# Kernel tuning notes

Hardware: AMD Instinct MI355X
Metric: run time of the kernel (lower is better)

## Reference

```python
import jax, jax.numpy as jnp
import numpy as np

N_NODES = 50000
N_EDGES = 1600000


def _gcn_conv(x, src, dst, W, b, num_nodes):
    # PyG GCNConv: out = D^-1/2 (A + I) D^-1/2 (x W) + b
    h = x @ W  # transform first (in_channels >= out_channels)
    deg = jax.ops.segment_sum(jnp.ones_like(dst, dtype=h.dtype), dst,
                              num_segments=num_nodes)
    dinv = jax.lax.rsqrt(deg)  # deg >= 1 thanks to self-loops
    norm = dinv[src] * dinv[dst]  # [E+N]
    msg = h[src] * norm[:, None]  # gather + scale
    out = jax.ops.segment_sum(msg, dst, num_segments=num_nodes)
    return out + b


def setup_inputs() -> dict:
    key = jax.random.key(0)
    k1, k2, k3, k4 = jax.random.split(key, 4)
    x = jax.random.normal(k1, (N_NODES, 512), dtype=jnp.float32)
    edge_index = jax.random.randint(k2, (2, N_EDGES), 0, N_NODES, dtype=jnp.int64)
    # Glorot-ish init for the two GCNConv weights
    W1 = jax.random.normal(k3, (512, 128), dtype=jnp.float32) * (1.0 / np.sqrt(512))
    b1 = jnp.zeros((128,), dtype=jnp.float32)
    W2 = jax.random.normal(k4, (128, 64), dtype=jnp.float32) * (1.0 / np.sqrt(128))
    b2 = jnp.zeros((64,), dtype=jnp.float32)
    return {"x": x, "edge_index": edge_index, "W1": W1, "b1": b1,
            "W2": W2, "b2": b2}


def reference(x, edge_index, W1, b1, W2, b2):
    num_nodes = x.shape[0]
    loop = jnp.arange(num_nodes, dtype=edge_index.dtype)
    src = jnp.concatenate([edge_index[0], loop])  # add self-loops
    dst = jnp.concatenate([edge_index[1], loop])
    h = jax.nn.relu(_gcn_conv(x, src, dst, W1, b1, num_nodes))
    out = _gcn_conv(h, src, dst, W2, b2, num_nodes)
    return out
```

## Files before the change

### kernel.cpp

```cpp
#include <hip/hip_runtime.h>
#include <hip/hip_bf16.h>


typedef __attribute__((ext_vector_type(8))) short short8;
typedef __attribute__((ext_vector_type(4))) float f32x4;

#define BSHIFT 9
#define BSIZE 512
constexpr int NBMAX = 128;
constexpr int CAP = 32768;
constexpr int CHUNK = 4096;

__device__ __forceinline__ unsigned short bf16_bits(float f) {
  __hip_bfloat16 h = __float2bfloat16(f);
  return *(unsigned short*)&h;
}
__device__ __forceinline__ float bf16_f(unsigned short u) {
  __hip_bfloat16 h = *(__hip_bfloat16*)&u;
  return __bfloat162float(h);
}
__device__ __forceinline__ void gload_lds16(const void* g, void* l) {
  __builtin_amdgcn_global_load_lds(
      (const __attribute__((address_space(1))) unsigned*)g,
      (__attribute__((address_space(3))) unsigned*)l, 16, 0, 0);
}
__device__ __forceinline__ int edge_at(const void* p, long long i, int is64) {
  return is64 ? (int)((const long long*)p)[i] : ((const int*)p)[i];
}

__global__ __launch_bounds__(256) void k_binA(
    const void* __restrict__ eidx, int* __restrict__ ccur,
    unsigned* __restrict__ pairs,
    const float* __restrict__ W1, unsigned short* __restrict__ W1h,
    unsigned short* __restrict__ W1l,
    const float* __restrict__ W2, unsigned short* __restrict__ W2h,
    unsigned short* __restrict__ W2l, int E, int NB, int nchunks) {
  const int tid = threadIdx.x;
  if ((int)blockIdx.x >= nchunks) {
    int o = ((int)blockIdx.x - nchunks) * 256 + tid;
    const float* W; unsigned short *Wh, *Wl; int Nn;
    if (o < 512 * 128) { W = W1; Wh = W1h; Wl = W1l; Nn = 128; }
    else { o -= 512 * 128; if (o >= 128 * 64) return;
           W = W2; Wh = W2h; Wl = W2l; Nn = 64; }
    int e = o & 7;
    int fm = (o >> 3) & 15;
    int fq = (o >> 7) & 3;
    int rest = o >> 9;
    int nt16 = Nn >> 4;
    int jt = rest % nt16;
    int t = rest / nt16;
    int k = t * 32 + fq * 8 + e;
    int n = jt * 16 + fm;
    float w = W[(long long)k * Nn + n];
    unsigned short hb = bf16_bits(w);
    Wh[o] = hb;
    Wl[o] = bf16_bits(w - bf16_f(hb));
    return;
  }
  __shared__ int s_nz;
  __shared__ int cnt[NBMAX];
  __shared__ int scn[NBMAX + 1];
  __shared__ int cur[NBMAX];
  __shared__ int gbase[NBMAX];
  __shared__ unsigned out[CHUNK];
  if (tid == 0) s_nz = 0;
  for (int b = tid; b < NBMAX; b += 256) cnt[b] = 0;
  __syncthreads();
  {
    int nz = 0;
    for (int i = 1 + 2 * tid; i < 4096; i += 512)
      nz |= (((const int*)eidx)[i] != 0);
    if (nz) atomicOr(&s_nz, 1);
  }
  __syncthreads();
  const int is64 = (s_nz == 0) ? 1 : 0;
  const int cs = blockIdx.x * CHUNK;
  const int n = min(CHUNK, E - cs);
  unsigned pk[CHUNK / 256];
#pragma unroll
  for (int it = 0; it < CHUNK / 256; ++it) {
    int i = cs + it * 256 + tid;
    unsigned p = 0xFFFFFFFFu;
    if (i < E) {
      int s = edge_at(eidx, i, is64);
      int d = edge_at(eidx, (long long)E + i, is64);
      p = ((unsigned)d << 16) | (unsigned)s;
      atomicAdd(&cnt[d >> BSHIFT], 1);
    }
    pk[it] = p;
  }
  __syncthreads();
  if (tid < NB) scn[tid + 1] = cnt[tid];
  if (tid == 0) scn[0] = 0;
  __syncthreads();
  for (int off = 1; off < NB; off <<= 1) {
    int t = 0;
    if (tid < NB && tid + 1 > off) t = scn[tid + 1 - off];
    __syncthreads();
    if (tid < NB && tid + 1 > off) scn[tid + 1] += t;
    __syncthreads();
  }
  if (tid < NB) {
    cur[tid] = scn[tid];
    gbase[tid] = (cnt[tid] > 0)
        ? (tid * CAP + atomicAdd(&ccur[tid], cnt[tid])) : 0;
  }
  __syncthreads();
#pragma unroll
  for (int it = 0; it < CHUNK / 256; ++it) {
    unsigned p = pk[it];
    if (p != 0xFFFFFFFFu) {
      int b = (int)(p >> (16 + BSHIFT));
      int pos = atomicAdd(&cur[b], 1);
      out[pos] = p;
    }
  }
  __syncthreads();
  for (int p2 = tid; p2 < n; p2 += 256) {
    unsigned v = out[p2];
    int b = (int)(v >> (16 + BSHIFT));
    pairs[gbase[b] + (p2 - scn[b])] = v;
  }
}

__global__ __launch_bounds__(256) void k_binB(
    const unsigned* __restrict__ pairs, const int* __restrict__ ccur,
    int* __restrict__ rowptr, float* __restrict__ dinv,
    unsigned short* __restrict__ elist, int N, int NB, int E) {
  __shared__ int scn2[NBMAX];
  __shared__ int hist[BSIZE];
  __shared__ int loc[BSIZE];
  const int b = blockIdx.x;
  const int tid = threadIdx.x;
  if (b == 0 && tid == 0) rowptr[N] = E;
  if (tid < NBMAX) scn2[tid] = (tid < NB) ? ccur[tid] : 0;
  __syncthreads();
  for (int off = 1; off < NBMAX; off <<= 1) {
    int t = (tid < NBMAX && tid >= off) ? scn2[tid - off] : 0;
    __syncthreads();
    if (tid < NBMAX) scn2[tid] += t;
    __syncthreads();
  }
  const int cntb = ccur[b];
  const int base = scn2[b] - cntb;
  const int nbeg = b * CAP;
  const int j0 = tid, j1 = tid + 256;
  hist[j0] = 0; hist[j1] = 0;
  __syncthreads();
  for (int i = tid; i < cntb; i += 256) {
    unsigned v = pairs[nbeg + i];
    atomicAdd(&hist[(v >> 16) & (BSIZE - 1)], 1);
  }
  __syncthreads();
  loc[j0] = hist[j0]; loc[j1] = hist[j1];
  __syncthreads();
  for (int off = 1; off < BSIZE; off <<= 1) {
    int v0 = (j0 >= off) ? loc[j0 - off] : 0;
    int v1 = (j1 >= off) ? loc[j1 - off] : 0;
    __syncthreads();
    loc[j0] += v0; loc[j1] += v1;
    __syncthreads();
  }
  int c0 = base + loc[j0] - hist[j0];
  int c1 = base + loc[j1] - hist[j1];
  int gd0 = b * BSIZE + j0, gd1 = b * BSIZE + j1;
  if (gd0 < N) { rowptr[gd0] = c0; dinv[gd0] = rsqrtf((float)(hist[j0] + 1)); }
  if (gd1 < N) { rowptr[gd1] = c1; dinv[gd1] = rsqrtf((float)(hist[j1] + 1)); }
  __syncthreads();
  hist[j0] = c0; hist[j1] = c1;
  __syncthreads();
  for (int i = tid; i < cntb; i += 256) {
    unsigned v = pairs[nbeg + i];
    int pos = atomicAdd(&hist[(v >> 16) & (BSIZE - 1)], 1);
    elist[pos] = (unsigned short)(v & 0xFFFFu);
  }
}

template <int K, int NOUT, int WM, int WY, int WX, int TB>
__global__ __launch_bounds__(TB) void k_gemm_mfma(
    const float* __restrict__ X, const unsigned short* __restrict__ Whi,
    const unsigned short* __restrict__ Wlo, const float* __restrict__ dinv,
    unsigned short* __restrict__ Hs, int M) {
  constexpr int BM = WM * WY;
  constexpr int BN = 64 * WX;
  constexpr int KC = 32;
  constexpr int I = WM / 16;
  constexpr int NK = K / KC;
  constexpr int CH = BN * 4;
  static_assert(WY * WX * 64 == TB, "wave grid covers block");
  static_assert(BN == NOUT, "block covers full N");
  __shared__ unsigned short Bh[2][BN * KC], Bl[2][BN * KC];
  const int tid = threadIdx.x;
  const int lane = tid & 63, wv = tid >> 6;
  const int wy = wv / WX, wx = wv % WX;
  const int fm = lane & 15;
  const int fq = lane >> 4;
  const int base = blockIdx.x * BM;

  f32x4 acc[I][4];
#pragma unroll
  for (int i = 0; i < I; ++i)
#pragma unroll
    for (int j = 0; j < 4; ++j) acc[i][j] = (f32x4){0.f, 0.f, 0.f, 0.f};

  float4 av[2][I][2];

  auto loadA = [&](int k0, int pb) {
#pragma unroll
    for (int i = 0; i < I; ++i) {
      int row = base + wy * WM + i * 16 + fm;
      av[pb][i][0] = make_float4(0.f, 0.f, 0.f, 0.f);
      av[pb][i][1] = make_float4(0.f, 0.f, 0.f, 0.f);
      if (row < M) {
        const float4* p = (const float4*)&X[(long long)row * K + k0 + fq * 8];
        av[pb][i][0] = p[0];
        av[pb][i][1] = p[1];
      }
    }
  };
  auto issueB = [&](int t, int buf) {
#pragma unroll
    for (int it = 0; it < (CH + TB - 1) / TB; ++it) {
      int cb = it * TB + wv * 64;
      if (cb < CH) {
        size_t so = (size_t)t * (BN * 32) + (size_t)(cb + lane) * 8;
        gload_lds16(&Whi[so], (unsigned short*)&Bh[buf][0] + (size_t)cb * 8);
        gload_lds16(&Wlo[so], (unsigned short*)&Bl[buf][0] + (size_t)cb * 8);
      }
    }
  };
  auto cvt8 = [&](const float4& a, const float4& b, short8& h, short8& l) {
    float f0 = a.x, f1 = a.y, f2 = a.z, f3 = a.w;
    float f4 = b.x, f5 = b.y, f6 = b.z, f7 = b.w;
    unsigned short hb;
    hb = bf16_bits(f0); h[0] = (short)hb; l[0] = (short)bf16_bits(f0 - bf16_f(hb));
    hb = bf16_bits(f1); h[1] = (short)hb; l[1] = (short)bf16_bits(f1 - bf16_f(hb));
    hb = bf16_bits(f2); h[2] = (short)hb; l[2] = (short)bf16_bits(f2 - bf16_f(hb));
    hb = bf16_bits(f3); h[3] = (short)hb; l[3] = (short)bf16_bits(f3 - bf16_f(hb));
    hb = bf16_bits(f4); h[4] = (short)hb; l[4] = (short)bf16_bits(f4 - bf16_f(hb));
    hb = bf16_bits(f5); h[5] = (short)hb; l[5] = (short)bf16_bits(f5 - bf16_f(hb));
    hb = bf16_bits(f6); h[6] = (short)hb; l[6] = (short)bf16_bits(f6 - bf16_f(hb));
    hb = bf16_bits(f7); h[7] = (short)hb; l[7] = (short)bf16_bits(f7 - bf16_f(hb));
  };

  issueB(0, 0);
  loadA(0, 0);
  __syncthreads();

#pragma unroll 2
  for (int t = 0; t < NK; ++t) {
    const int pb = t & 1;
    if (t + 1 < NK) {
      issueB(t + 1, pb ^ 1);
      loadA((t + 1) * KC, pb ^ 1);
    }
    short8 ah[I], al[I];
#pragma unroll
    for (int i = 0; i < I; ++i) cvt8(av[pb][i][0], av[pb][i][1], ah[i], al[i]);
    short8 bh[4], bl[4];
#pragma unroll
    for (int j = 0; j < 4; ++j) {
      int jt = wx * 4 + j;
      bh[j] = *(const short8*)&Bh[pb][jt * 512 + lane * 8];
      bl[j] = *(const short8*)&Bl[pb][jt * 512 + lane * 8];
    }
#pragma unroll
    for (int i = 0; i < I; ++i)
#pragma unroll
      for (int j = 0; j < 4; ++j) {
        acc[i][j] = __builtin_amdgcn_mfma_f32_16x16x32_bf16(ah[i], bh[j], acc[i][j], 0, 0, 0);
        acc[i][j] = __builtin_amdgcn_mfma_f32_16x16x32_bf16(ah[i], bl[j], acc[i][j], 0, 0, 0);
        acc[i][j] = __builtin_amdgcn_mfma_f32_16x16x32_bf16(al[i], bh[j], acc[i][j], 0, 0, 0);
      }
    __syncthreads();
  }

#pragma unroll
  for (int i = 0; i < I; ++i) {
#pragma unroll
    for (int reg = 0; reg < 4; ++reg) {
      int row = base + wy * WM + i * 16 + fq * 4 + reg;
      if (row < M) {
        float dv = dinv[row];
#pragma unroll
        for (int j = 0; j < 4; ++j)
          Hs[(long long)row * NOUT + wx * 64 + j * 16 + fm] =
              bf16_bits(acc[i][j][reg] * dv);
      }
    }
  }
}

__device__ __forceinline__ void acc8(float* a, uint4 u) {
  const unsigned* p = (const unsigned*)&u;
#pragma unroll
  for (int q = 0; q < 4; ++q) {
    unsigned w = p[q];
    a[2 * q]     += __uint_as_float(w << 16);
    a[2 * q + 1] += __uint_as_float(w & 0xFFFF0000u);
  }
}

template <int C, bool RELU>
__global__ __launch_bounds__(256) void k_gather(
    const int* __restrict__ rowptr, const unsigned short* __restrict__ elist,
    const float* __restrict__ dinv, const unsigned short* __restrict__ Hs,
    const float* __restrict__ bias, float* __restrict__ OUT, int N) {
  constexpr int TPN = C / 8;
  constexpr int NPB = 256 / TPN;
  const int node = blockIdx.x * NPB + (int)threadIdx.x / TPN;
  const int lane = (int)threadIdx.x % TPN;
  if (node >= N) return;
  const int col = lane * 8;
  const int beg = rowptr[node];
  const int end = rowptr[node + 1];
  float a0[8] = {0, 0, 0, 0, 0, 0, 0, 0};
  float a1[8] = {0, 0, 0, 0, 0, 0, 0, 0};
  acc8(a0, *(const uint4*)&Hs[(long long)node * C + col]);
  int e = beg;
  for (; e + 3 < end; e += 4) {
    int s0 = elist[e], s1 = elist[e + 1], s2 = elist[e + 2], s3 = elist[e + 3];
    uint4 v0 = *(const uint4*)&Hs[(long long)s0 * C + col];
    uint4 v1 = *(const uint4*)&Hs[(long long)s1 * C + col];
    uint4 v2 = *(const uint4*)&Hs[(long long)s2 * C + col];
    uint4 v3 = *(const uint4*)&Hs[(long long)s3 * C + col];
    acc8(a0, v0); acc8(a1, v1); acc8(a0, v2); acc8(a1, v3);
  }
  for (; e < end; ++e) {
    uint4 v0 = *(const uint4*)&Hs[(long long)elist[e] * C + col];
    acc8(a0, v0);
  }
  const float dv = dinv[node];
  float o[8];
#pragma unroll
  for (int i = 0; i < 8; ++i) {
    o[i] = (a0[i] + a1[i]) * dv + bias[col + i];
    if (RELU) o[i] = fmaxf(o[i], 0.f);
  }
  *(float4*)&OUT[(long long)node * C + col] = make_float4(o[0], o[1], o[2], o[3]);
  *(float4*)&OUT[(long long)node * C + col + 4] = make_float4(o[4], o[5], o[6], o[7]);
}

extern "C" void kernel_launch(void* const* d_in, const int* in_sizes, int n_in,
                              void* d_out, int out_size, void* d_ws, size_t ws_size,
                              hipStream_t stream) {
  const float* x  = (const float*)d_in[0];
  const void*  ei = d_in[1];
  const float* W1 = (const float*)d_in[2];
  const float* b1 = (const float*)d_in[3];
  const float* W2 = (const float*)d_in[4];
  const float* b2 = (const float*)d_in[5];
  float* out = (float*)d_out;
  const int N = in_sizes[0] / 512;
  const int E = in_sizes[1] / 2;
  const int NB = (N + BSIZE - 1) >> BSHIFT;
  const int nchunks = (E + CHUNK - 1) / CHUNK;

  char* ws = (char*)d_ws;
  size_t off = 0;
  auto take = [&](size_t bytes) {
    void* p = ws + off;
    off = (off + bytes + 255) & ~(size_t)255;
    return p;
  };
  float* dinv   = (float*)take((size_t)N * 4);
  int*   rowptr = (int*)take((size_t)(N + 1) * 4);
  int*   ccur   = (int*)take((size_t)NBMAX * 4);
  unsigned short* elist = (unsigned short*)take((size_t)E * 2);
  unsigned short* Wt1h = (unsigned short*)take((size_t)512 * 128 * 2);
  unsigned short* Wt1l = (unsigned short*)take((size_t)512 * 128 * 2);
  unsigned short* Wt2h = (unsigned short*)take((size_t)128 * 64 * 2);
  unsigned short* Wt2l = (unsigned short*)take((size_t)128 * 64 * 2);
  unsigned short* Hs = (unsigned short*)take((size_t)N * 128 * 2);
  float* h2     = (float*)take((size_t)N * 128 * 4);
  unsigned short* Hs2 = Hs;
  unsigned* pairs = (unsigned*)h2;

  const int B = 256;
  constexpr int WJOBS = (512 * 128 + 128 * 64) / 256;
  hipMemsetAsync(ccur, 0, (size_t)NBMAX * 4, stream);
  k_binA<<<nchunks + WJOBS, B, 0, stream>>>(ei, ccur, pairs,
                                            W1, Wt1h, Wt1l, W2, Wt2h, Wt2l,
                                            E, NB, nchunks);
  k_binB<<<NB, B, 0, stream>>>(pairs, ccur, rowptr, dinv, elist, N, NB, E);
  k_gemm_mfma<512, 128, 32, 4, 2, 512><<<(N + 127) / 128, 512, 0, stream>>>(
      x, Wt1h, Wt1l, dinv, Hs, N);
  k_gather<128, true><<<(N + 15) / 16, B, 0, stream>>>(rowptr, elist, dinv, Hs, b1, h2, N);
  k_gemm_mfma<128, 64, 32, 4, 1, 256><<<(N + 127) / 128, 256, 0, stream>>>(
      h2, Wt2h, Wt2l, dinv, Hs2, N);
  k_gather<64, false><<<(N + 31) / 32, B, 0, stream>>>(rowptr, elist, dinv, Hs2, b2, out, N);
}
```

Baseline: 322.5 us.

## Fuse layer-1 gather with layer-2 GEMM through shared memory

Adds a kernel that aggregates 64 nodes' layer-1 neighbor features with bias and ReLU, then splits the result into bf16 hi/lo parts and stores them in swizzled LDS. The layer-2 MFMA GEMM runs straight from that LDS tile. This drops the fp32 h2 intermediate round trip through global memory and one launch. In exchange, the gather loses parallelism (16 threads per node over 4 rounds, 64 nodes per block), B fragments are read directly from global memory, and the pairs and Hs2 buffers now get their own workspace allocations.

```diff
diff --git a/kernel.cpp b/kernel.cpp
--- a/kernel.cpp
+++ b/kernel.cpp
@@ -301,6 +301,98 @@
   }
 }
 
+template <int C, int COUT>
+__global__ __launch_bounds__(256) void k_gather_gemm(
+    const int* __restrict__ rowptr, const unsigned short* __restrict__ elist,
+    const float* __restrict__ dinv, const unsigned short* __restrict__ Hs,
+    const float* __restrict__ bias,
+    const unsigned short* __restrict__ W2h,
+    const unsigned short* __restrict__ W2l,
+    unsigned short* __restrict__ Hs2, int N) {
+  constexpr int NT = C / 32;
+  static_assert(C == 128 && COUT == 64, "fused shape");
+  __shared__ unsigned short Ah[64 * C], Al[64 * C];
+  const int tid = threadIdx.x;
+  const int lane16 = tid & 15;
+  const int rl0 = tid >> 4;
+
+  const int nb = blockIdx.x * 64;
+
+  for (int rnd = 0; rnd < 4; ++rnd) {
+    const int r = rnd * 16 + rl0;
+    const int node = nb + r;
+    short8 h = (short8){0, 0, 0, 0, 0, 0, 0, 0};
+    short8 l = h;
+    if (node < N) {
+      const int col = lane16 * 8;
+      const int beg = rowptr[node];
+      const int end = rowptr[node + 1];
+      float a0[8] = {0, 0, 0, 0, 0, 0, 0, 0};
+      float a1[8] = {0, 0, 0, 0, 0, 0, 0, 0};
+      acc8(a0, *(const uint4*)&Hs[(long long)node * C + col]);
+      int e = beg;
+      for (; e + 3 < end; e += 4) {
+        int s0 = elist[e], s1 = elist[e + 1];
+        int s2 = elist[e + 2], s3 = elist[e + 3];
+        uint4 v0 = *(const uint4*)&Hs[(long long)s0 * C + col];
+        uint4 v1 = *(const uint4*)&Hs[(long long)s1 * C + col];
+        uint4 v2 = *(const uint4*)&Hs[(long long)s2 * C + col];
+        uint4 v3 = *(const uint4*)&Hs[(long long)s3 * C + col];
+        acc8(a0, v0); acc8(a1, v1); acc8(a0, v2); acc8(a1, v3);
+      }
+      for (; e < end; ++e) {
+        uint4 v0 = *(const uint4*)&Hs[(long long)elist[e] * C + col];
+        acc8(a0, v0);
+      }
+      const float dv = dinv[node];
+#pragma unroll
+      for (int i = 0; i < 8; ++i) {
+        float o = (a0[i] + a1[i]) * dv + bias[col + i];
+        o = fmaxf(o, 0.f);
+        unsigned short hb = bf16_bits(o);
+        h[i] = (short)hb;
+        l[i] = (short)bf16_bits(o - bf16_f(hb));
+      }
+    }
+    const int widx = r * C + ((lane16 ^ (r & 7)) * 8);
+    *(short8*)&Ah[widx] = h;
+    *(short8*)&Al[widx] = l;
+  }
+  __syncthreads();
+
+  const int lane = tid & 63, wv = tid >> 6;
+  const int fm = lane & 15, fq = lane >> 4;
+  f32x4 acc[4];
+#pragma unroll
+  for (int j = 0; j < 4; ++j) acc[j] = (f32x4){0.f, 0.f, 0.f, 0.f};
+#pragma unroll
+  for (int t = 0; t < NT; ++t) {
+    const int aidx = (wv * 16 + fm) * C + (((t * 4 + fq) ^ (fm & 7)) * 8);
+    short8 ah = *(const short8*)&Ah[aidx];
+    short8 al = *(const short8*)&Al[aidx];
+#pragma unroll
+    for (int j = 0; j < 4; ++j) {
+      const int so = (t * 4 + j) * 512 + lane * 8;
+      short8 bh = *(const short8*)&W2h[so];
+      short8 bl = *(const short8*)&W2l[so];
+      acc[j] = __builtin_amdgcn_mfma_f32_16x16x32_bf16(ah, bh, acc[j], 0, 0, 0);
+      acc[j] = __builtin_amdgcn_mfma_f32_16x16x32_bf16(ah, bl, acc[j], 0, 0, 0);
+      acc[j] = __builtin_amdgcn_mfma_f32_16x16x32_bf16(al, bh, acc[j], 0, 0, 0);
+    }
+  }
+#pragma unroll
+  for (int reg = 0; reg < 4; ++reg) {
+    const int row = nb + wv * 16 + fq * 4 + reg;
+    if (row < N) {
+      const float dv = dinv[row];
+#pragma unroll
+      for (int j = 0; j < 4; ++j)
+        Hs2[(long long)row * COUT + j * 16 + fm] =
+            bf16_bits(acc[j][reg] * dv);
+    }
+  }
+}
+
 template <int C, bool RELU>
 __global__ __launch_bounds__(256) void k_gather(
     const int* __restrict__ rowptr, const unsigned short* __restrict__ elist,
@@ -371,10 +463,9 @@
   unsigned short* Wt1l = (unsigned short*)take((size_t)512 * 128 * 2);
   unsigned short* Wt2h = (unsigned short*)take((size_t)128 * 64 * 2);
   unsigned short* Wt2l = (unsigned short*)take((size_t)128 * 64 * 2);
-  unsigned short* Hs = (unsigned short*)take((size_t)N * 128 * 2);
-  float* h2     = (float*)take((size_t)N * 128 * 4);
-  unsigned short* Hs2 = Hs;
-  unsigned* pairs = (unsigned*)h2;
+  unsigned short* Hs  = (unsigned short*)take((size_t)N * 128 * 2);
+  unsigned short* Hs2 = (unsigned short*)take((size_t)N * 64 * 2);
+  unsigned* pairs = (unsigned*)take((size_t)NBMAX * CAP * 4);
 
   const int B = 256;
   constexpr int WJOBS = (512 * 128 + 128 * 64) / 256;
@@ -385,8 +476,7 @@
   k_binB<<<NB, B, 0, stream>>>(pairs, ccur, rowptr, dinv, elist, N, NB, E);
   k_gemm_mfma<512, 128, 32, 4, 2, 512><<<(N + 127) / 128, 512, 0, stream>>>(
       x, Wt1h, Wt1l, dinv, Hs, N);
-  k_gather<128, true><<<(N + 15) / 16, B, 0, stream>>>(rowptr, elist, dinv, Hs, b1, h2, N);
-  k_gemm_mfma<128, 64, 32, 4, 1, 256><<<(N + 127) / 128, 256, 0, stream>>>(
-      h2, Wt2h, Wt2l, dinv, Hs2, N);
+  k_gather_gemm<128, 64><<<(N + 63) / 64, B, 0, stream>>>(
+      rowptr, elist, dinv, Hs, b1, Wt2h, Wt2l, Hs2, N);
   k_gather<64, false><<<(N + 31) / 32, B, 0, stream>>>(rowptr, elist, dinv, Hs2, b2, out, N);
 }
```

After: 318.7 us. Within noise of the previous version (-1.2%).
